# Kernel tuning notes

Measured on AMD Instinct MI355X. Metric: run time of the kernel, lower is better.

Reference implementation:

```python
import jax, jax.numpy as jnp
import numpy as np

NUM_HEADS = 16
NUM_KV_GROUPS = 4
EPS = 1e-6


def _rms_norm(x, w):
    # normalize over last dim (head_dim)
    return x * jax.lax.rsqrt(jnp.mean(x * x, axis=-1, keepdims=True) + EPS) * w


def _rope_cos_sin(T, head_dim):
    half = head_dim // 2
    inv_freq = 1.0 / (10000.0 ** (jnp.arange(half, dtype=jnp.float32) / half))
    freqs = jnp.arange(T, dtype=jnp.float32)[:, None] * inv_freq[None, :]  # [T, half]
    cos = jnp.repeat(jnp.cos(freqs), 2, axis=-1)  # [T, head_dim]
    sin = jnp.repeat(jnp.sin(freqs), 2, axis=-1)
    return cos, sin


def _apply_rope(x, cos, sin):
    # x: [B, H, T, head_dim]; cos/sin broadcast over B,H
    x1 = x[..., ::2]
    x2 = x[..., 1::2]
    x_rot = jnp.stack([-x2, x1], axis=-1).reshape(x.shape)  # interleave (-x2, x1)
    return x * cos + x_rot * sin


def setup_inputs() -> dict:
    key = jax.random.key(0)
    ks = jax.random.split(key, 5)
    scale = lambda k, sh: jax.random.normal(k, sh, dtype=jnp.float32) * 0.02
    return {
        "x": jax.random.normal(ks[0], (4, 2048, 1024), dtype=jnp.float32),
        "Wq": scale(ks[1], (1024, 1024)),
        "Wk": scale(ks[2], (256, 1024)),
        "Wv": scale(ks[3], (256, 1024)),
        "Wo": scale(ks[4], (1024, 1024)),
        "qn_w": jnp.ones((64,), jnp.float32),
        "kn_w": jnp.ones((64,), jnp.float32),
    }


def reference(x, Wq, Wk, Wv, Wo, qn_w, kn_w):
    B, T, D = x.shape
    H, G = NUM_HEADS, NUM_KV_GROUPS
    hd = D // H

    # projections (torch Linear: y = x @ W.T), reshape to [B, heads, T, hd]
    q = (x @ Wq.T).reshape(B, T, H, hd).transpose(0, 2, 1, 3)
    k = (x @ Wk.T).reshape(B, T, G, hd).transpose(0, 2, 1, 3)
    v = (x @ Wv.T).reshape(B, T, G, hd).transpose(0, 2, 1, 3)

    # optional qk RMSNorm (qk_norm=True)
    q = _rms_norm(q, qn_w)
    k = _rms_norm(k, kn_w)

    # RoPE (position_offset = 0)
    cos, sin = _rope_cos_sin(T, hd)
    q = _apply_rope(q, cos, sin)
    k = _apply_rope(k, cos, sin)

    # GQA: expand kv heads to match query heads
    rep = H // G
    k = jnp.repeat(k, rep, axis=1)
    v = jnp.repeat(v, rep, axis=1)

    # causal SDPA
    scores = jnp.einsum('bhqd,bhkd->bhqk', q, k) / jnp.sqrt(jnp.float32(hd))
    causal = jnp.tril(jnp.ones((T, T), dtype=bool))
    scores = jnp.where(causal, scores, jnp.float32(-1e30))
    attn = jax.nn.softmax(scores, axis=-1)
    out = jnp.einsum('bhqk,bhkd->bhqd', attn, v)

    out = out.transpose(0, 2, 1, 3).reshape(B, T, D)
    return out @ Wo.T
```

## Files before the change

kernel.cpp:

```cpp
#include <hip/hip_runtime.h>

typedef unsigned short u16;
typedef __attribute__((ext_vector_type(8))) short bf16x8;
typedef __attribute__((ext_vector_type(4))) short bf16x4;
typedef __attribute__((ext_vector_type(4))) float f32x4;

#define GP(p) ((const __attribute__((address_space(1))) void*)(unsigned long long)(p))
#define LP(p) ((__attribute__((address_space(3))) void*)(unsigned int)(unsigned long long)(p))

#define QSCALE 0.180336879486998f
#define M_BIAS (-12.0f)

__device__ __forceinline__ u16 f2bf(float f) {
  union { float f; unsigned u; } v; v.f = f;
  unsigned r = v.u + 0x7fffu + ((v.u >> 16) & 1u);
  return (u16)(r >> 16);
}
__device__ __forceinline__ short f2bf_cvt(float f) {
  __bf16 b = (__bf16)f;
  return *reinterpret_cast<short*>(&b);
}

#if __has_builtin(__builtin_amdgcn_mfma_f32_16x16x16bf16_1k)
#define MFMA16(A, B, C) __builtin_amdgcn_mfma_f32_16x16x16bf16_1k((A), (B), (C), 0, 0, 0)
#elif __has_builtin(__builtin_amdgcn_mfma_f32_16x16x16_bf16)
#define MFMA16(A, B, C) __builtin_amdgcn_mfma_f32_16x16x16_bf16((A), (B), (C), 0, 0, 0)
#else
static __device__ __forceinline__ f32x4 mfma16_asm(bf16x4 a, bf16x4 b, f32x4 c) {
  asm volatile("v_mfma_f32_16x16x16_bf16 %0, %1, %2, %0" : "+v"(c) : "v"(a), "v"(b));
  return c;
}
#define MFMA16(A, B, C) mfma16_asm((A), (B), (C))
#endif

__global__ void prep_kernel(const float* __restrict__ x,
                            const float* __restrict__ Wq, const float* __restrict__ Wk,
                            const float* __restrict__ Wv, const float* __restrict__ Wo,
                            u16* __restrict__ xb, u16* __restrict__ Wcat,
                            u16* __restrict__ Wob,
                            float* __restrict__ ctab, float* __restrict__ stab) {
  const int bid = blockIdx.x, tid = threadIdx.x;
  if (bid < 2048) {
    for (int i = bid * 256 + tid; i < 2097152; i += 2048 * 256) {
      float4 v = reinterpret_cast<const float4*>(x)[i];
      reinterpret_cast<ushort4*>(xb)[i] =
          make_ushort4(f2bf(v.x), f2bf(v.y), f2bf(v.z), f2bf(v.w));
    }
  } else if (bid < 2688) {
    for (int i = (bid - 2048) * 256 + tid; i < 655360; i += 640 * 256) {
      const float* src; u16* dst; int off;
      if (i < 262144)      { src = Wq; dst = Wcat;           off = i; }
      else if (i < 327680) { src = Wk; dst = Wcat + 1048576; off = i - 262144; }
      else if (i < 393216) { src = Wv; dst = Wcat + 1310720; off = i - 327680; }
      else                 { src = Wo; dst = Wob;            off = i - 393216; }
      float4 v = reinterpret_cast<const float4*>(src)[off];
      reinterpret_cast<ushort4*>(dst)[off] =
          make_ushort4(f2bf(v.x), f2bf(v.y), f2bf(v.z), f2bf(v.w));
    }
  } else {
    int i = (bid - 2688) * 256 + tid;
    int t = i >> 5, f = i & 31;
    float inv = exp2f((float)f * (-13.287712379549449f / 32.0f));
    float ang = (float)t * inv;
    float sv, cv;
    sincosf(ang, &sv, &cv);
    ctab[i] = cv;
    stab[i] = sv;
  }
}

__launch_bounds__(256)
__global__ void gemm_qkv_kernel(const u16* __restrict__ A, const u16* __restrict__ W,
                                u16* __restrict__ qh, u16* __restrict__ kh,
                                u16* __restrict__ vt,
                                const float* __restrict__ qn_w, const float* __restrict__ kn_w,
                                const float* __restrict__ ctab, const float* __restrict__ stab) {
  __shared__ __align__(16) u16 As[128 * 64];
  __shared__ __align__(16) u16 Bs[128 * 64];
  const int tid = threadIdx.x;
  const int w = tid >> 6, l = tid & 63;
  const int lr = l & 15, lk = l >> 4;
  const int wr = w >> 1, wc = w & 1;
  const int m0 = blockIdx.x * 128, n0 = blockIdx.y * 128;
  f32x4 acc[4][4] = {};
  for (int k0 = 0; k0 < 1024; k0 += 64) {
#pragma unroll
    for (int i = 0; i < 4; ++i) {
      int c = i * 256 + tid;
      const u16* ga = A + (size_t)(m0 + (c >> 3)) * 1024 + k0 + (c & 7) * 8;
      __builtin_amdgcn_global_load_lds(GP(ga), LP((char*)As + (i * 256 + (tid & ~63)) * 16), 16, 0, 0);
      const u16* gb = W + (size_t)(n0 + (c >> 3)) * 1024 + k0 + (c & 7) * 8;
      __builtin_amdgcn_global_load_lds(GP(gb), LP((char*)Bs + (i * 256 + (tid & ~63)) * 16), 16, 0, 0);
    }
    asm volatile("s_waitcnt vmcnt(0)" ::: "memory");
    __syncthreads();
#pragma unroll
    for (int kk = 0; kk < 2; ++kk) {
      bf16x8 af[4], bfr[4];
#pragma unroll
      for (int fi = 0; fi < 4; ++fi)
        af[fi] = *reinterpret_cast<const bf16x8*>(&As[(wr * 64 + fi * 16 + lr) * 64 + kk * 32 + lk * 8]);
#pragma unroll
      for (int fj = 0; fj < 4; ++fj)
        bfr[fj] = *reinterpret_cast<const bf16x8*>(&Bs[(wc * 64 + fj * 16 + lr) * 64 + kk * 32 + lk * 8]);
#pragma unroll
      for (int fi = 0; fi < 4; ++fi)
#pragma unroll
        for (int fj = 0; fj < 4; ++fj)
          acc[fi][fj] = __builtin_amdgcn_mfma_f32_16x16x32_bf16(af[fi], bfr[fj], acc[fi][fj], 0, 0, 0);
    }
    __syncthreads();
  }
  const int ncol0 = n0 + wc * 64;
  if (ncol0 < 1280) {
    const bool isq = ncol0 < 1024;
    const float* wn = isq ? qn_w : kn_w;
    const float sc = isq ? QSCALE : 1.0f;
    float wv[4];
#pragma unroll
    for (int fj = 0; fj < 4; ++fj) wv[fj] = wn[fj * 16 + lr];
#pragma unroll
    for (int fi = 0; fi < 4; ++fi)
#pragma unroll
      for (int r = 0; r < 4; ++r) {
        float ss = 0.f;
#pragma unroll
        for (int fj = 0; fj < 4; ++fj) ss += acc[fi][fj][r] * acc[fi][fj][r];
        ss += __shfl_xor(ss, 1); ss += __shfl_xor(ss, 2);
        ss += __shfl_xor(ss, 4); ss += __shfl_xor(ss, 8);
        float rinv = rsqrtf(ss * (1.0f / 64.0f) + 1e-6f);
        int m = m0 + wr * 64 + fi * 16 + lk * 4 + r;
        int t = m & 2047, b = m >> 11;
#pragma unroll
        for (int fj = 0; fj < 4; ++fj) {
          float xn = acc[fi][fj][r] * rinv * wv[fj];
          float pr = __shfl_xor(xn, 1);
          float rot = (lr & 1) ? pr : -pr;
          int ci = t * 32 + fj * 8 + (lr >> 1);
          u16 outv = f2bf((xn * ctab[ci] + rot * stab[ci]) * sc);
          int n = ncol0 + fj * 16 + lr;
          if (isq) {
            int h = n >> 6, d = n & 63;
            qh[((size_t)((b * 16 + h) * 2048 + t)) * 64 + d] = outv;
          } else {
            int n2 = n - 1024, g = n2 >> 6, d = n2 & 63;
            kh[((size_t)((b * 4 + g) * 2048 + t)) * 64 + d] = outv;
          }
        }
      }
  } else {
#pragma unroll
    for (int fi = 0; fi < 4; ++fi)
#pragma unroll
      for (int fj = 0; fj < 4; ++fj) {
        int m = m0 + wr * 64 + fi * 16 + lk * 4;
        int b = m >> 11, t = m & 2047;
        int n2 = ncol0 + fj * 16 + lr - 1280;
        int g = n2 >> 6, d = n2 & 63;
        bf16x4 o;
#pragma unroll
        for (int r = 0; r < 4; ++r) o[r] = f2bf_cvt(acc[fi][fj][r]);
        *reinterpret_cast<bf16x4*>(&vt[((size_t)((b * 4 + g) * 64 + d)) * 2048 + t]) = o;
      }
  }
}

__launch_bounds__(512)
__global__ void attn_kernel(const u16* __restrict__ qh, const u16* __restrict__ kh,
                            const u16* __restrict__ vt, u16* __restrict__ ao) {
  __shared__ __align__(16) u16 Ks[2][64 * 64];
  __shared__ __align__(16) u16 Vts[2][64 * 64];
  const int tid = threadIdx.x, w = tid >> 6, l = tid & 63;
  const int lr = l & 15, lk = l >> 4;
  const int wq = w & 3, wh = w >> 2;
  const int D = blockIdx.x;
  const int j = D >> 3;
  const int p = j & 15, hp = (j >> 4) & 1;
  const int z = (D & 7) + 8 * (j >> 5);
  const int b = z >> 2, g = z & 3;
  const int h = g * 4 + hp * 2 + wh;
  const u16* Qh = qh + ((size_t)((b * 16 + h) * 2048)) * 64;
  const u16* Kb = kh + ((size_t)z * 2048) * 64;
  const u16* Vtb = vt + ((size_t)z * 64) * 2048;
  const int swz = (lr & 7) * 8;

  const int r0 = tid >> 3, s0 = ((tid & 7) ^ (r0 & 7)) * 8;
  char* kd = (char*)&Ks[0][0] + (tid & ~63) * 16;
  char* vd = (char*)&Vts[0][0] + (tid & ~63) * 16;
  const u16* kp; const u16* vp;

  auto stage = [&](int buf) {
    __builtin_amdgcn_global_load_lds(GP(kp), LP(kd + buf * 8192), 16, 0, 0);
    __builtin_amdgcn_global_load_lds(GP(vp), LP(vd + buf * 8192), 16, 0, 0);
    kp += 64 * 64; vp += 64;
  };

  int cur = 0;
  auto run_qtile = [&](int qt) {
    const int q0 = qt * 64;
    const u16* Qb = Qh + (size_t)(q0 + wq * 16) * 64;
    const bf16x8 qf0 = *reinterpret_cast<const bf16x8*>(&Qb[lr * 64 + lk * 8]);
    const bf16x8 qf1 = *reinterpret_cast<const bf16x8*>(&Qb[lr * 64 + 32 + lk * 8]);
    f32x4 oacc[4] = {};
    float lrow = 0.f;
    kp = Kb + r0 * 64 + s0;
    vp = Vtb + (size_t)r0 * 2048 + s0;
    stage(cur);
    asm volatile("s_waitcnt vmcnt(0)" ::: "memory");
    __builtin_amdgcn_s_barrier();
    for (int it = 0; it <= qt; ++it) {
      if (it < qt) stage(cur ^ 1);
      f32x4 sacc[4];
#pragma unroll
      for (int fi = 0; fi < 4; ++fi)
#pragma unroll
        for (int r = 0; r < 4; ++r) sacc[fi][r] = M_BIAS;
      __builtin_amdgcn_s_setprio(1);
#pragma unroll
      for (int kk = 0; kk < 2; ++kk) {
        bf16x8 qf = kk ? qf1 : qf0;
#pragma unroll
        for (int fi = 0; fi < 4; ++fi) {
          bf16x8 kf = *reinterpret_cast<const bf16x8*>(
              &Ks[cur][(fi * 16 + lr) * 64 + ((kk * 32 + lk * 8) ^ swz)]);
          sacc[fi] = __builtin_amdgcn_mfma_f32_16x16x32_bf16(kf, qf, sacc[fi], 0, 0, 0);
        }
      }
      __builtin_amdgcn_s_setprio(0);
      if (it == qt) {
        int qloc = wq * 16 + lr;
#pragma unroll
        for (int fi = 0; fi < 4; ++fi)
#pragma unroll
          for (int r = 0; r < 4; ++r)
            if (fi * 16 + lk * 4 + r > qloc) sacc[fi][r] = -1e30f;
      }
      bf16x4 pb[4];
#pragma unroll
      for (int fi = 0; fi < 4; ++fi)
#pragma unroll
        for (int r = 0; r < 4; ++r) {
          float pv = exp2f(sacc[fi][r]);
          lrow += pv;
          pb[fi][r] = f2bf_cvt(pv);
        }
      __builtin_amdgcn_s_setprio(1);
#pragma unroll
      for (int fi = 0; fi < 4; ++fi)
#pragma unroll
        for (int db = 0; db < 4; ++db) {
          bf16x4 vf = *reinterpret_cast<const bf16x4*>(
              &Vts[cur][(db * 16 + lr) * 64 + ((fi * 16 + lk * 4) ^ swz)]);
          oacc[db] = MFMA16(vf, pb[fi], oacc[db]);
        }
      __builtin_amdgcn_s_setprio(0);
      asm volatile("s_waitcnt vmcnt(0)" ::: "memory");
      __builtin_amdgcn_s_barrier();
      cur ^= 1;
    }
    float lsum = lrow;
    lsum += __shfl_xor(lsum, 16);
    lsum += __shfl_xor(lsum, 32);
    float inv = 1.0f / lsum;
#pragma unroll
    for (int db = 0; db < 4; ++db) {
      bf16x4 o;
#pragma unroll
      for (int r = 0; r < 4; ++r) o[r] = f2bf_cvt(oacc[db][r] * inv);
      *reinterpret_cast<bf16x4*>(
          &ao[((size_t)(b * 2048 + q0 + wq * 16 + lr)) * 1024 + h * 64 + db * 16 + lk * 4]) = o;
    }
  };
  run_qtile(31 - p);
  run_qtile(p);
}

__launch_bounds__(256)
__global__ void gemm_out_kernel(const u16* __restrict__ A, const u16* __restrict__ W,
                                float* __restrict__ out) {
  __shared__ __align__(16) u16 As[2][128 * 64];
  __shared__ __align__(16) u16 Bs[2][128 * 64];
  const int tid = threadIdx.x;
  const int w = tid >> 6, l = tid & 63;
  const int lr = l & 15, lk = l >> 4;
  const int wr = w >> 1, wc = w & 1;
  const int m0 = blockIdx.x * 128, n0 = blockIdx.y * 128;
  const u16* ap[4];
  const u16* bp[4];
#pragma unroll
  for (int i = 0; i < 4; ++i) {
    int c = i * 256 + tid;
    ap[i] = A + (size_t)(m0 + (c >> 3)) * 1024 + (c & 7) * 8;
    bp[i] = W + (size_t)(n0 + (c >> 3)) * 1024 + (c & 7) * 8;
  }
  auto stage = [&](int buf) {
#pragma unroll
    for (int i = 0; i < 4; ++i) {
      __builtin_amdgcn_global_load_lds(GP(ap[i]),
          LP((char*)&As[0][0] + buf * 16384 + (i * 256 + (tid & ~63)) * 16), 16, 0, 0);
      __builtin_amdgcn_global_load_lds(GP(bp[i]),
          LP((char*)&Bs[0][0] + buf * 16384 + (i * 256 + (tid & ~63)) * 16), 16, 0, 0);
      ap[i] += 64; bp[i] += 64;
    }
  };
  f32x4 acc[4][4] = {};
  int cur = 0;
  stage(0);
  asm volatile("s_waitcnt vmcnt(0)" ::: "memory");
  __builtin_amdgcn_s_barrier();
  for (int k0 = 0; k0 < 1024; k0 += 64) {
    if (k0 < 960) stage(cur ^ 1);
    __builtin_amdgcn_s_setprio(1);
#pragma unroll
    for (int kk = 0; kk < 2; ++kk) {
      bf16x8 af[4], bfr[4];
#pragma unroll
      for (int fi = 0; fi < 4; ++fi)
        af[fi] = *reinterpret_cast<const bf16x8*>(
            &As[cur][(wr * 64 + fi * 16 + lr) * 64 + kk * 32 + lk * 8]);
#pragma unroll
      for (int fj = 0; fj < 4; ++fj)
        bfr[fj] = *reinterpret_cast<const bf16x8*>(
            &Bs[cur][(wc * 64 + fj * 16 + lr) * 64 + kk * 32 + lk * 8]);
#pragma unroll
      for (int fi = 0; fi < 4; ++fi)
#pragma unroll
        for (int fj = 0; fj < 4; ++fj)
          acc[fi][fj] = __builtin_amdgcn_mfma_f32_16x16x32_bf16(af[fi], bfr[fj], acc[fi][fj], 0, 0, 0);
    }
    __builtin_amdgcn_s_setprio(0);
    asm volatile("s_waitcnt vmcnt(0)" ::: "memory");
    __builtin_amdgcn_s_barrier();
    cur ^= 1;
  }
#pragma unroll
  for (int fi = 0; fi < 4; ++fi)
#pragma unroll
    for (int fj = 0; fj < 4; ++fj)
#pragma unroll
      for (int r = 0; r < 4; ++r) {
        int m = m0 + wr * 64 + fi * 16 + lk * 4 + r;
        int n = n0 + wc * 64 + fj * 16 + lr;
        out[(size_t)m * 1024 + n] = acc[fi][fj][r];
      }
}

extern "C" void kernel_launch(void* const* d_in, const int* in_sizes, int n_in,
                              void* d_out, int out_size, void* d_ws, size_t ws_size,
                              hipStream_t stream) {
  const float* x  = (const float*)d_in[0];
  const float* Wq = (const float*)d_in[1];
  const float* Wk = (const float*)d_in[2];
  const float* Wv = (const float*)d_in[3];
  const float* Wo = (const float*)d_in[4];
  const float* qn = (const float*)d_in[5];
  const float* kn = (const float*)d_in[6];
  float* out = (float*)d_out;
  char* ws = (char*)d_ws;
  u16* xb   = (u16*)(ws);
  u16* Wcat = (u16*)(ws + 16777216);
  u16* Wob  = (u16*)(ws + 19922944);
  u16* qh   = (u16*)(ws + 22020096);
  u16* kh   = (u16*)(ws + 38797312);
  u16* vtb  = (u16*)(ws + 42991616);
  u16* ao   = (u16*)(ws + 47185920);
  float* ctab = (float*)ao;
  float* stab = ctab + 65536;

  prep_kernel<<<2944, 256, 0, stream>>>(x, Wq, Wk, Wv, Wo, xb, Wcat, Wob, ctab, stab);
  dim3 g1(64, 12);
  gemm_qkv_kernel<<<g1, 256, 0, stream>>>(xb, Wcat, qh, kh, vtb, qn, kn, ctab, stab);
  attn_kernel<<<512, 512, 0, stream>>>(qh, kh, vtb, ao);
  dim3 g2(64, 8);
  gemm_out_kernel<<<g2, 256, 0, stream>>>(ao, Wob, out);
}
```

Before: 165.3 us.

## Double-buffer QKV GEMM loads and widen attention KV tiles to 128

Splits the QKV projection GEMM's shared-memory tiles into two buffers, so the next K-slice is prefetched while MFMAs run on the current one. This replaces the previous load-wait-compute serialization. The attention kernel now processes 128 keys per iteration instead of 64, which halves the number of barriers and iterations, and raises its launch bounds to 4 blocks. The M_BIAS exponent offset is also removed, which changes the numeric range of the unnormalized exp2 values and doubles LDS use per block. A 64-key masking tail is handled by masking the last 128-wide tile.

```diff
diff --git a/kernel.cpp b/kernel.cpp
--- a/kernel.cpp
+++ b/kernel.cpp
@@ -9,7 +9,6 @@
 #define LP(p) ((__attribute__((address_space(3))) void*)(unsigned int)(unsigned long long)(p))
 
 #define QSCALE 0.180336879486998f
-#define M_BIAS (-12.0f)
 
 __device__ __forceinline__ u16 f2bf(float f) {
   union { float f; unsigned u; } v; v.f = f;
@@ -75,41 +74,60 @@
                                 u16* __restrict__ vt,
                                 const float* __restrict__ qn_w, const float* __restrict__ kn_w,
                                 const float* __restrict__ ctab, const float* __restrict__ stab) {
-  __shared__ __align__(16) u16 As[128 * 64];
-  __shared__ __align__(16) u16 Bs[128 * 64];
+  __shared__ __align__(16) u16 As[2][128 * 64];
+  __shared__ __align__(16) u16 Bs[2][128 * 64];
   const int tid = threadIdx.x;
   const int w = tid >> 6, l = tid & 63;
   const int lr = l & 15, lk = l >> 4;
   const int wr = w >> 1, wc = w & 1;
   const int m0 = blockIdx.x * 128, n0 = blockIdx.y * 128;
+  const u16* ap[4];
+  const u16* bp[4];
+#pragma unroll
+  for (int i = 0; i < 4; ++i) {
+    int c = i * 256 + tid;
+    ap[i] = A + (size_t)(m0 + (c >> 3)) * 1024 + (c & 7) * 8;
+    bp[i] = W + (size_t)(n0 + (c >> 3)) * 1024 + (c & 7) * 8;
+  }
+  auto stage = [&](int buf) {
+#pragma unroll
+    for (int i = 0; i < 4; ++i) {
+      __builtin_amdgcn_global_load_lds(GP(ap[i]),
+          LP((char*)&As[0][0] + buf * 16384 + (i * 256 + (tid & ~63)) * 16), 16, 0, 0);
+      __builtin_amdgcn_global_load_lds(GP(bp[i]),
+          LP((char*)&Bs[0][0] + buf * 16384 + (i * 256 + (tid & ~63)) * 16), 16, 0, 0);
+      ap[i] += 64; bp[i] += 64;
+    }
+  };
   f32x4 acc[4][4] = {};
+  int cur = 0;
+  stage(0);
+  asm volatile("s_waitcnt vmcnt(0)" ::: "memory");
+  __builtin_amdgcn_s_barrier();
   for (int k0 = 0; k0 < 1024; k0 += 64) {
-#pragma unroll
-    for (int i = 0; i < 4; ++i) {
-      int c = i * 256 + tid;
-      const u16* ga = A + (size_t)(m0 + (c >> 3)) * 1024 + k0 + (c & 7) * 8;
-      __builtin_amdgcn_global_load_lds(GP(ga), LP((char*)As + (i * 256 + (tid & ~63)) * 16), 16, 0, 0);
-      const u16* gb = W + (size_t)(n0 + (c >> 3)) * 1024 + k0 + (c & 7) * 8;
-      __builtin_amdgcn_global_load_lds(GP(gb), LP((char*)Bs + (i * 256 + (tid & ~63)) * 16), 16, 0, 0);
-    }
-    asm volatile("s_waitcnt vmcnt(0)" ::: "memory");
-    __syncthreads();
+    if (k0 < 960) stage(cur ^ 1);
+    __builtin_amdgcn_s_setprio(1);
 #pragma unroll
     for (int kk = 0; kk < 2; ++kk) {
       bf16x8 af[4], bfr[4];
 #pragma unroll
       for (int fi = 0; fi < 4; ++fi)
-        af[fi] = *reinterpret_cast<const bf16x8*>(&As[(wr * 64 + fi * 16 + lr) * 64 + kk * 32 + lk * 8]);
+        af[fi] = *reinterpret_cast<const bf16x8*>(
+            &As[cur][(wr * 64 + fi * 16 + lr) * 64 + kk * 32 + lk * 8]);
 #pragma unroll
       for (int fj = 0; fj < 4; ++fj)
-        bfr[fj] = *reinterpret_cast<const bf16x8*>(&Bs[(wc * 64 + fj * 16 + lr) * 64 + kk * 32 + lk * 8]);
+        bfr[fj] = *reinterpret_cast<const bf16x8*>(
+            &Bs[cur][(wc * 64 + fj * 16 + lr) * 64 + kk * 32 + lk * 8]);
 #pragma unroll
       for (int fi = 0; fi < 4; ++fi)
 #pragma unroll
         for (int fj = 0; fj < 4; ++fj)
           acc[fi][fj] = __builtin_amdgcn_mfma_f32_16x16x32_bf16(af[fi], bfr[fj], acc[fi][fj], 0, 0, 0);
     }
-    __syncthreads();
+    __builtin_amdgcn_s_setprio(0);
+    asm volatile("s_waitcnt vmcnt(0)" ::: "memory");
+    __builtin_amdgcn_s_barrier();
+    cur ^= 1;
   }
   const int ncol0 = n0 + wc * 64;
   if (ncol0 < 1280) {
@@ -165,11 +183,11 @@
   }
 }
 
-__launch_bounds__(512)
+__launch_bounds__(512, 4)
 __global__ void attn_kernel(const u16* __restrict__ qh, const u16* __restrict__ kh,
                             const u16* __restrict__ vt, u16* __restrict__ ao) {
-  __shared__ __align__(16) u16 Ks[2][64 * 64];
-  __shared__ __align__(16) u16 Vts[2][64 * 64];
+  __shared__ __align__(16) u16 Ks[2][128 * 64];
+  __shared__ __align__(16) u16 Vts[2][64 * 128];
   const int tid = threadIdx.x, w = tid >> 6, l = tid & 63;
   const int lr = l & 15, lk = l >> 4;
   const int wq = w & 3, wh = w >> 2;
@@ -184,75 +202,84 @@
   const u16* Vtb = vt + ((size_t)z * 64) * 2048;
   const int swz = (lr & 7) * 8;
 
-  const int r0 = tid >> 3, s0 = ((tid & 7) ^ (r0 & 7)) * 8;
+  const int kr = tid >> 3;
+  const int ksrc = ((tid & 7) ^ (kr & 7)) * 8;
+  const int vr = tid >> 4, vx = tid & 15;
+  const int vsrc = (vx >> 3) * 64 + (((vx & 7) ^ (vr & 7)) * 8);
   char* kd = (char*)&Ks[0][0] + (tid & ~63) * 16;
   char* vd = (char*)&Vts[0][0] + (tid & ~63) * 16;
   const u16* kp; const u16* vp;
 
   auto stage = [&](int buf) {
-    __builtin_amdgcn_global_load_lds(GP(kp), LP(kd + buf * 8192), 16, 0, 0);
-    __builtin_amdgcn_global_load_lds(GP(vp), LP(vd + buf * 8192), 16, 0, 0);
-    kp += 64 * 64; vp += 64;
+    __builtin_amdgcn_global_load_lds(GP(kp), LP(kd + buf * 16384), 16, 0, 0);
+    __builtin_amdgcn_global_load_lds(GP(kp + 64 * 64), LP(kd + buf * 16384 + 8192), 16, 0, 0);
+    __builtin_amdgcn_global_load_lds(GP(vp), LP(vd + buf * 16384), 16, 0, 0);
+    __builtin_amdgcn_global_load_lds(GP(vp + 32 * 2048), LP(vd + buf * 16384 + 8192), 16, 0, 0);
+    kp += 128 * 64; vp += 128;
   };
 
   int cur = 0;
   auto run_qtile = [&](int qt) {
     const int q0 = qt * 64;
+    const int nIt = (qt + 2) >> 1;
     const u16* Qb = Qh + (size_t)(q0 + wq * 16) * 64;
     const bf16x8 qf0 = *reinterpret_cast<const bf16x8*>(&Qb[lr * 64 + lk * 8]);
     const bf16x8 qf1 = *reinterpret_cast<const bf16x8*>(&Qb[lr * 64 + 32 + lk * 8]);
     f32x4 oacc[4] = {};
     float lrow = 0.f;
-    kp = Kb + r0 * 64 + s0;
-    vp = Vtb + (size_t)r0 * 2048 + s0;
+    kp = Kb + kr * 64 + ksrc;
+    vp = Vtb + (size_t)vr * 2048 + vsrc;
     stage(cur);
     asm volatile("s_waitcnt vmcnt(0)" ::: "memory");
     __builtin_amdgcn_s_barrier();
-    for (int it = 0; it <= qt; ++it) {
-      if (it < qt) stage(cur ^ 1);
-      f32x4 sacc[4];
-#pragma unroll
-      for (int fi = 0; fi < 4; ++fi)
-#pragma unroll
-        for (int r = 0; r < 4; ++r) sacc[fi][r] = M_BIAS;
+    for (int it = 0; it < nIt; ++it) {
+      if (it + 1 < nIt) stage(cur ^ 1);
+      f32x4 sacc[2][4] = {};
       __builtin_amdgcn_s_setprio(1);
 #pragma unroll
-      for (int kk = 0; kk < 2; ++kk) {
-        bf16x8 qf = kk ? qf1 : qf0;
-#pragma unroll
-        for (int fi = 0; fi < 4; ++fi) {
-          bf16x8 kf = *reinterpret_cast<const bf16x8*>(
-              &Ks[cur][(fi * 16 + lr) * 64 + ((kk * 32 + lk * 8) ^ swz)]);
-          sacc[fi] = __builtin_amdgcn_mfma_f32_16x16x32_bf16(kf, qf, sacc[fi], 0, 0, 0);
+      for (int hf = 0; hf < 2; ++hf)
+#pragma unroll
+        for (int kk = 0; kk < 2; ++kk) {
+          bf16x8 qf = kk ? qf1 : qf0;
+#pragma unroll
+          for (int fi = 0; fi < 4; ++fi) {
+            bf16x8 kf = *reinterpret_cast<const bf16x8*>(
+                &Ks[cur][(hf * 64 + fi * 16 + lr) * 64 + ((kk * 32 + lk * 8) ^ swz)]);
+            sacc[hf][fi] = __builtin_amdgcn_mfma_f32_16x16x32_bf16(kf, qf, sacc[hf][fi], 0, 0, 0);
+          }
         }
+      __builtin_amdgcn_s_setprio(0);
+      if (it == nIt - 1) {
+        const int Dq = ((qt & 1) ? 64 : 0) + wq * 16 + lr;
+#pragma unroll
+        for (int hf = 0; hf < 2; ++hf)
+#pragma unroll
+          for (int fi = 0; fi < 4; ++fi)
+#pragma unroll
+            for (int r = 0; r < 4; ++r)
+              if (hf * 64 + fi * 16 + lk * 4 + r > Dq) sacc[hf][fi][r] = -1e30f;
       }
-      __builtin_amdgcn_s_setprio(0);
-      if (it == qt) {
-        int qloc = wq * 16 + lr;
+      __builtin_amdgcn_s_setprio(1);
+#pragma unroll
+      for (int hf = 0; hf < 2; ++hf) {
+        bf16x4 pb[4];
 #pragma unroll
         for (int fi = 0; fi < 4; ++fi)
 #pragma unroll
-          for (int r = 0; r < 4; ++r)
-            if (fi * 16 + lk * 4 + r > qloc) sacc[fi][r] = -1e30f;
+          for (int r = 0; r < 4; ++r) {
+            float pv = exp2f(sacc[hf][fi][r]);
+            lrow += pv;
+            pb[fi][r] = f2bf_cvt(pv);
+          }
+#pragma unroll
+        for (int fi = 0; fi < 4; ++fi)
+#pragma unroll
+          for (int db = 0; db < 4; ++db) {
+            bf16x4 vf = *reinterpret_cast<const bf16x4*>(
+                &Vts[cur][(db * 16 + lr) * 128 + hf * 64 + ((fi * 16 + lk * 4) ^ swz)]);
+            oacc[db] = MFMA16(vf, pb[fi], oacc[db]);
+          }
       }
-      bf16x4 pb[4];
-#pragma unroll
-      for (int fi = 0; fi < 4; ++fi)
-#pragma unroll
-        for (int r = 0; r < 4; ++r) {
-          float pv = exp2f(sacc[fi][r]);
-          lrow += pv;
-          pb[fi][r] = f2bf_cvt(pv);
-        }
-      __builtin_amdgcn_s_setprio(1);
-#pragma unroll
-      for (int fi = 0; fi < 4; ++fi)
-#pragma unroll
-        for (int db = 0; db < 4; ++db) {
-          bf16x4 vf = *reinterpret_cast<const bf16x4*>(
-              &Vts[cur][(db * 16 + lr) * 64 + ((fi * 16 + lk * 4) ^ swz)]);
-          oacc[db] = MFMA16(vf, pb[fi], oacc[db]);
-        }
       __builtin_amdgcn_s_setprio(0);
       asm volatile("s_waitcnt vmcnt(0)" ::: "memory");
       __builtin_amdgcn_s_barrier();
```

Measured after the change: 155.2 us. 6.1% less time.
